# Optimization experiments

Measured on AMD Instinct MI355X. Metric: run time of the kernel, lower is better.

The kernel has to match this reference:

```python
import jax, jax.numpy as jnp
import numpy as np

NUM_HEADS = 16
ROPE_BASE = 10000.0

def rotate_half(x):
    h = x.shape[-1] // 2
    return jnp.concatenate([-x[..., h:], x[..., :h]], axis=-1)

def setup_inputs() -> dict:
    key = jax.random.key(0)
    k1, k2, k3, k4 = jax.random.split(key, 4)
    B, T, H = 2, 2048, 1024
    hidden_state = jax.random.normal(k1, (B, T, H), dtype=jnp.float32)
    # right-padding mask: per-batch valid lengths
    lengths = jnp.array([2048, 1536], dtype=jnp.int32)
    attention_mask = (jnp.arange(T, dtype=jnp.int32)[None, :] < lengths[:, None]).astype(jnp.int32)
    s = 1.0 / np.sqrt(H)
    w_qkv = jax.random.normal(k2, (H, 3 * H), dtype=jnp.float32) * s
    b_qkv = jax.random.normal(k3, (3 * H,), dtype=jnp.float32) * 0.01
    w_out = jax.random.normal(k4, (H, H), dtype=jnp.float32) * s
    return {"hidden_state": hidden_state, "attention_mask": attention_mask,
            "w_qkv": w_qkv, "b_qkv": b_qkv, "w_out": w_out}

def reference(hidden_state, attention_mask, w_qkv, b_qkv, w_out):
    B, T, H = hidden_state.shape
    hd = H // NUM_HEADS
    qkv = hidden_state @ w_qkv + b_qkv                      # [B,T,3H]
    qkv = qkv.reshape(B, T, NUM_HEADS, 3 * hd).swapaxes(1, 2)  # [B,h,T,3d]
    q, k, v = qkv[..., :hd], qkv[..., hd:2 * hd], qkv[..., 2 * hd:]
    # rotary embedding (cache computed in fp32, as in torch module)
    inv_freq = 1.0 / (ROPE_BASE ** (jnp.arange(0, hd, 2, dtype=jnp.float32) / hd))
    t = jnp.arange(T, dtype=jnp.float32)
    freqs = jnp.outer(t, inv_freq)                          # [T, hd/2]
    emb = jnp.concatenate([freqs, freqs], axis=-1)          # [T, hd]
    cos = jnp.cos(emb)[None, None]                          # [1,1,T,hd]
    sin = jnp.sin(emb)[None, None]
    q = q * cos + rotate_half(q) * sin
    k = k * cos + rotate_half(k) * sin
    scale = 1.0 / jnp.sqrt(jnp.asarray(hd, dtype=q.dtype))
    scores = jnp.einsum('bhqd,bhkd->bhqk', q, k) * scale    # [B,h,T,T]
    causal = jnp.triu(jnp.ones((T, T), dtype=bool), k=1)    # True = masked (future)
    pad = (attention_mask == 0)[:, None, None, :]           # True = masked (padded key)
    mask = causal[None, None] | pad
    scores = jnp.where(mask, jnp.finfo(scores.dtype).min, scores)
    attn = jax.nn.softmax(scores, axis=-1)
    out = jnp.einsum('bhqk,bhkd->bhqd', attn, v)            # [B,h,T,d]
    out = out.swapaxes(1, 2).reshape(B, T, H)
    return out @ w_out
```

## Files before the change

### kernel.cpp

```cpp
#include <hip/hip_runtime.h>
#include <math.h>

typedef __attribute__((ext_vector_type(8))) short short8;
typedef __attribute__((ext_vector_type(4))) short short4v;
typedef __attribute__((ext_vector_type(4))) float floatx4;

#define T_SEQ 2048
#define NHEADS 16
#define HID 1024

#if __has_builtin(__builtin_amdgcn_mfma_f32_16x16x16bf16_1k)
#define MFMA16(a,b,c) __builtin_amdgcn_mfma_f32_16x16x16bf16_1k(a,b,c,0,0,0)
#elif __has_builtin(__builtin_amdgcn_mfma_f32_16x16x16_bf16)
#define MFMA16(a,b,c) __builtin_amdgcn_mfma_f32_16x16x16_bf16(a,b,c,0,0,0)
#else
#define MFMA16(a,b,c) (c)
#endif

#if __has_builtin(__builtin_amdgcn_exp2f)
#define EXP2F(x) __builtin_amdgcn_exp2f(x)
#else
#define EXP2F(x) exp2f(x)
#endif

__device__ __forceinline__ ushort f2b(float x){
  union { float f; unsigned u; } c; c.f = x;
  unsigned r = c.u + 0x7fffu + ((c.u >> 16) & 1u);
  return (ushort)(r >> 16);
}

__device__ __forceinline__ floatx4 fzero4(){
  floatx4 v; v[0]=0.f; v[1]=0.f; v[2]=0.f; v[3]=0.f; return v;
}

__device__ __forceinline__ void gl_lds16(const ushort* g, ushort* l){
  __builtin_amdgcn_global_load_lds(
      (const __attribute__((address_space(1))) void*)g,
      (__attribute__((address_space(3))) void*)l, 16, 0, 0);
}


__global__ __launch_bounds__(256) void prep(
    const float* __restrict__ hidden, const float* __restrict__ w_qkv,
    const float* __restrict__ w_out, const int* __restrict__ amask,
    ushort* __restrict__ hO, ushort* __restrict__ wqkvT, ushort* __restrict__ woutT,
    float2* __restrict__ cs, int* __restrict__ Lb)
{
  __shared__ __align__(16) char smem[32 * 33 * 4];
  int blk = blockIdx.x;
  int tid = threadIdx.x;

  if (blk < 4096){
    int i = blk * 256 + tid;
    float4 v = ((const float4*)hidden)[i];
    ushort4 o;
    o.x = f2b(v.x); o.y = f2b(v.y); o.z = f2b(v.z); o.w = f2b(v.w);
    ((ushort4*)hO)[i] = o;
  } else if (blk < 8192){
    const float* in; ushort* out; int R, C, bx, by;
    if (blk < 7168){
      int t = blk - 4096; bx = t % 96; by = t / 96;
      in = w_qkv; out = wqkvT; R = 1024; C = 3072;
    } else {
      int t = blk - 7168; bx = t & 31; by = t >> 5;
      in = w_out; out = woutT; R = 1024; C = 1024;
    }
    float (*tile)[33] = (float(*)[33])smem;
    int c0 = bx * 32, r0 = by * 32;
    int tx = tid & 31, ty = tid >> 5;
    #pragma unroll
    for (int i = 0; i < 4; i++){
      int r = ty + i * 8;
      tile[r][tx] = in[(size_t)(r0 + r) * C + c0 + tx];
    }
    __syncthreads();
    #pragma unroll
    for (int i = 0; i < 4; i++){
      int r = ty + i * 8;
      out[(size_t)(c0 + r) * R + r0 + tx] = f2b(tile[tx][r]);
    }
  } else if (blk < 8448){
    int idx = (blk - 8192) * 256 + tid;
    int t = idx >> 5, i = idx & 31;
    float invf = powf(10000.0f, -(float)i / 32.0f);
    float a = (float)t * invf;
    cs[idx] = make_float2(cosf(a), sinf(a));
  } else {
    int b = blk - 8448;
    int* red = (int*)smem;
    int s = 0;
    for (int i = tid; i < T_SEQ; i += 256) s += amask[b * T_SEQ + i];
    red[tid] = s; __syncthreads();
    for (int o = 128; o > 0; o >>= 1){
      if (tid < o) red[tid] += red[tid + o];
      __syncthreads();
    }
    if (tid == 0) Lb[b] = red[0];
  }
}


__global__ __launch_bounds__(768, 3) void gemm_qkv(
    const ushort* __restrict__ A, const ushort* __restrict__ Bt,
    const float* __restrict__ bias,
    ushort* __restrict__ qO, ushort* __restrict__ kO, ushort* __restrict__ vT,
    const float2* __restrict__ cs)
{
  __shared__ __align__(16) ushort As[3 * 16384];
  __shared__ __align__(16) ushort Bs[2 * 12288];
  int tid = threadIdx.x;
  int bid = blockIdx.x;
  int swz = (bid & 7) * 32 + (bid >> 3);
  int bm = swz >> 4, bn = swz & 15;
  int wave = tid >> 6, lane = tid & 63;
  int wm = wave & 3, wn = wave >> 2;
  int quad = lane >> 4, l15 = lane & 15, l7 = lane & 7;

  int lr3 = lane >> 3, sl = lane & 7;
  int gsl = sl ^ lr3;
  const ushort* gA = A  + (size_t)(bm * 256 + wave * 8 + lr3) * 1024 + (gsl << 3);
  const ushort* gB = Bt + (size_t)(bn * 192 + (wave - 8) * 8 + lr3) * 1024 + (gsl << 3);

  auto stageA = [&](int slot, int kt2){
    #pragma unroll
    for (int i = 0; i < 4; i++)
      gl_lds16(gA + (size_t)(i * 64) * 1024 + kt2 * 64,
               &As[slot * 16384 + i * 4096 + wave * 512]);
  };
  auto stageB = [&](int slot, int kt2){
    #pragma unroll
    for (int i = 0; i < 6; i++)
      gl_lds16(gB + (size_t)(i * 32) * 1024 + kt2 * 64,
               &Bs[slot * 12288 + i * 2048 + (wave - 8) * 512]);
  };

  int s0 = (quad ^ l7) << 3;
  int s1 = ((quad + 4) ^ l7) << 3;

  floatx4 acc[4][4];
  #pragma unroll
  for (int i = 0; i < 4; i++)
    #pragma unroll
    for (int j = 0; j < 4; j++) acc[i][j] = fzero4();

  if (tid < 512){ stageA(0, 0); stageA(1, 1); }
  else          { stageB(0, 0); }

  int aCur = 0, aStage = 2, bCur = 0;

  for (int kt = 0; kt < 16; ++kt){
    if (tid < 512){
      if (kt < 15) asm volatile("s_waitcnt vmcnt(4)" ::: "memory");
      else         asm volatile("s_waitcnt vmcnt(0)" ::: "memory");
    } else {
      asm volatile("s_waitcnt vmcnt(0)" ::: "memory");
    }
    __builtin_amdgcn_s_barrier();

    const ushort* Ac = &As[aCur * 16384];
    const ushort* Bc = &Bs[bCur * 12288];

    short8 af[4][2], bfr[2][2];
    #pragma unroll
    for (int mt = 0; mt < 4; mt++){
      int ro = (wm * 64 + mt * 16 + l15) * 64;
      af[mt][0] = *(const short8*)&Ac[ro + s0];
      af[mt][1] = *(const short8*)&Ac[ro + s1];
    }
    #pragma unroll
    for (int nt = 0; nt < 2; nt++){
      int ro = (wn * 64 + nt * 16 + l15) * 64;
      bfr[nt][0] = *(const short8*)&Bc[ro + s0];
      bfr[nt][1] = *(const short8*)&Bc[ro + s1];
    }
    if (tid < 512){ if (kt <= 13) stageA(aStage, kt + 2); }
    else          { if (kt <= 14) stageB(bCur ^ 1, kt + 1); }

    __builtin_amdgcn_s_setprio(1);
    #pragma unroll
    for (int mt = 0; mt < 4; mt++)
      #pragma unroll
      for (int nt = 0; nt < 2; nt++){
        acc[mt][nt] = __builtin_amdgcn_mfma_f32_16x16x32_bf16(af[mt][0], bfr[nt][0], acc[mt][nt], 0, 0, 0);
        acc[mt][nt] = __builtin_amdgcn_mfma_f32_16x16x32_bf16(af[mt][1], bfr[nt][1], acc[mt][nt], 0, 0, 0);
      }
    __builtin_amdgcn_s_setprio(0);

    short8 bfr2[2][2];
    #pragma unroll
    for (int nt = 0; nt < 2; nt++){
      int ro = (wn * 64 + (nt + 2) * 16 + l15) * 64;
      bfr2[nt][0] = *(const short8*)&Bc[ro + s0];
      bfr2[nt][1] = *(const short8*)&Bc[ro + s1];
    }
    __builtin_amdgcn_s_setprio(1);
    #pragma unroll
    for (int mt = 0; mt < 4; mt++)
      #pragma unroll
      for (int nt = 0; nt < 2; nt++){
        acc[mt][nt + 2] = __builtin_amdgcn_mfma_f32_16x16x32_bf16(af[mt][0], bfr2[nt][0], acc[mt][nt + 2], 0, 0, 0);
        acc[mt][nt + 2] = __builtin_amdgcn_mfma_f32_16x16x32_bf16(af[mt][1], bfr2[nt][1], acc[mt][nt + 2], 0, 0, 0);
      }
    __builtin_amdgcn_s_setprio(0);

    aCur   = (aCur   == 2) ? 0 : aCur + 1;
    aStage = (aStage == 2) ? 0 : aStage + 1;
    bCur ^= 1;
  }

  int g = bn * 3 + wn;
  int h = g / 3, comp = g - h * 3;

  if (comp == 2){
    #pragma unroll
    for (int nt = 0; nt < 4; nt++){
      int d = nt * 16 + l15;
      float bv = bias[g * 64 + d];
      #pragma unroll
      for (int mt = 0; mt < 4; mt++){
        int row = bm * 256 + wm * 64 + mt * 16 + quad * 4;
        int t = row & (T_SEQ - 1), b_ = row >> 11;
        ushort4 o;
        o.x = f2b(acc[mt][nt][0] + bv);
        o.y = f2b(acc[mt][nt][1] + bv);
        o.z = f2b(acc[mt][nt][2] + bv);
        o.w = f2b(acc[mt][nt][3] + bv);
        *(ushort4*)&vT[(size_t)((b_ * NHEADS + h) * 64 + d) * T_SEQ + t] = o;
      }
    }
  } else {
    ushort* outP = (comp == 0) ? qO : kO;
    float qs = (comp == 0) ? 0.125f * 1.44269504089f : 1.0f;
    float bv[4], bp[4];
    #pragma unroll
    for (int nt = 0; nt < 4; nt++){
      bv[nt] = bias[g * 64 + nt * 16 + l15];
      bp[nt] = bias[g * 64 + ((nt * 16 + l15) ^ 32)];
    }
    #pragma unroll
    for (int mt = 0; mt < 4; mt++)
      #pragma unroll
      for (int r = 0; r < 4; r++){
        int row = bm * 256 + wm * 64 + mt * 16 + quad * 4 + r;
        int t = row & (T_SEQ - 1), b_ = row >> 11;
        float2 c0 = cs[t * 32 + l15];
        float2 c1 = cs[t * 32 + 16 + l15];
        size_t base = (size_t)((b_ * NHEADS + h) * T_SEQ + t) * 64 + l15;
        #pragma unroll
        for (int nt = 0; nt < 4; nt++){
          float cvv = (nt & 1) ? c1.x : c0.x;
          float svv = (nt & 1) ? c1.y : c0.y;
          float sgn = (nt < 2) ? -1.0f : 1.0f;
          float val = acc[mt][nt][r] + bv[nt];
          float pv  = acc[mt][nt ^ 2][r] + bp[nt];
          outP[base + nt * 16] = f2b((val * cvv + sgn * pv * svv) * qs);
        }
      }
  }
}


__global__ __launch_bounds__(256) void attn(
    const ushort* __restrict__ qB, const ushort* __restrict__ kB,
    const ushort* __restrict__ vTB, const int* __restrict__ Lb,
    ushort* __restrict__ oB)
{
  __shared__ __align__(16) ushort SH[2][8192];
  int tid = threadIdx.x;
  int bh = blockIdx.x;
  int qt = 31 - blockIdx.y;
  int b = bh >> 4, h = bh & 15;
  int wave = tid >> 6, lane = tid & 63;
  int quad = lane >> 4, l15 = lane & 15;
  int q0 = qt * 64;
  int L = Lb[b];

  const ushort* Qb  = qB + (size_t)bh * T_SEQ * 64;
  const ushort* Kb  = kB + (size_t)bh * T_SEQ * 64;
  const ushort* VtB = vTB + (size_t)bh * 64 * T_SEQ;

  int qrow = q0 + wave * 16 + l15;
  short8 qf0 = *(const short8*)&Qb[(size_t)qrow * 64 + quad * 8];
  short8 qf1 = *(const short8*)&Qb[(size_t)qrow * 64 + 32 + quad * 8];

  int lr = lane >> 3, ch = lane & 7;
  int sw = (ch ^ lr) * 8;
  int l7 = l15 & 7;

  float l_i = 0.f;
  floatx4 oacc[4];
  #pragma unroll
  for (int nt = 0; nt < 4; nt++) oacc[nt] = fzero4();

  int lastkb = qt;
  int lkb2 = (L - 1) >> 6;
  if (lkb2 < lastkb) lastkb = lkb2;

  auto stageKV = [&](int kb, int buf){
    int k0 = kb * 64;
    const ushort* gK = &Kb[(size_t)(k0 + wave * 16 + lr) * 64 + sw];
    gl_lds16(gK,          &SH[buf][(wave * 16) * 64]);
    gl_lds16(gK + 8 * 64, &SH[buf][(wave * 16 + 8) * 64]);
    const ushort* gV = &VtB[(size_t)(wave * 16 + lr) * T_SEQ + k0 + sw];
    gl_lds16(gV,             &SH[buf][4096 + (wave * 16) * 64]);
    gl_lds16(gV + 8 * T_SEQ, &SH[buf][4096 + (wave * 16 + 8) * 64]);
  };

  stageKV(0, 0);
  __syncthreads();

  for (int kb = 0; kb <= lastkb; ++kb){
    int cur = kb & 1;
    if (kb < lastkb) stageKV(kb + 1, cur ^ 1);
    const ushort* Ks = &SH[cur][0];
    const ushort* Vt = &SH[cur][4096];
    int k0 = kb * 64;

    floatx4 sacc[4];
    #pragma unroll
    for (int e = 0; e < 4; e++){
      short8 kf0 = *(const short8*)&Ks[(e * 16 + l15) * 64 + ((quad ^ l7) * 8)];
      short8 kf1 = *(const short8*)&Ks[(e * 16 + l15) * 64 + (((quad | 4) ^ l7) * 8)];
      floatx4 z = fzero4();
      z = __builtin_amdgcn_mfma_f32_16x16x32_bf16(kf0, qf0, z, 0, 0, 0);
      z = __builtin_amdgcn_mfma_f32_16x16x32_bf16(kf1, qf1, z, 0, 0, 0);
      sacc[e] = z;
    }

    float p[4][4];
    bool needm = (kb == qt) || (k0 + 64 > L);
    if (needm){
      #pragma unroll
      for (int e = 0; e < 4; e++)
        #pragma unroll
        for (int r = 0; r < 4; r++){
          int key = k0 + e * 16 + quad * 4 + r;
          float ev = EXP2F(sacc[e][r]);
          p[e][r] = (key <= qrow && key < L) ? ev : 0.f;
        }
    } else {
      #pragma unroll
      for (int e = 0; e < 4; e++)
        #pragma unroll
        for (int r = 0; r < 4; r++) p[e][r] = EXP2F(sacc[e][r]);
    }
    float s0 = 0.f, s1 = 0.f, s2 = 0.f, s3 = 0.f;
    #pragma unroll
    for (int e = 0; e < 4; e++){
      s0 += p[e][0]; s1 += p[e][1]; s2 += p[e][2]; s3 += p[e][3];
    }
    l_i += (s0 + s1) + (s2 + s3);

    short4v pf[4];
    #pragma unroll
    for (int e = 0; e < 4; e++){
      union { unsigned u[2]; short4v v; } pk;
      pk.u[0] = (__float_as_uint(p[e][1]) & 0xffff0000u) | (__float_as_uint(p[e][0]) >> 16);
      pk.u[1] = (__float_as_uint(p[e][3]) & 0xffff0000u) | (__float_as_uint(p[e][2]) >> 16);
      pf[e] = pk.v;
    }

    #pragma unroll
    for (int nt = 0; nt < 4; nt++){
      #pragma unroll
      for (int e = 0; e < 4; e++){
        int cw = e * 2 + (quad >> 1);
        short4v vf = *(const short4v*)&Vt[(nt * 16 + l15) * 64 + ((cw ^ l7) * 8) + (quad & 1) * 4];
        oacc[nt] = MFMA16(vf, pf[e], oacc[nt]);
      }
    }
    __syncthreads();
  }

  l_i += __shfl_xor(l_i, 16);
  l_i += __shfl_xor(l_i, 32);
  float inv = 1.f / l_i;

  ushort (*Ot)[80] = (ushort(*)[80])&SH[0][0];
  #pragma unroll
  for (int nt = 0; nt < 4; nt++){
    ushort4 o;
    o.x = f2b(oacc[nt][0] * inv);
    o.y = f2b(oacc[nt][1] * inv);
    o.z = f2b(oacc[nt][2] * inv);
    o.w = f2b(oacc[nt][3] * inv);
    *(ushort4*)&Ot[wave * 16 + l15][nt * 16 + quad * 4] = o;
  }
  __syncthreads();
  int r = tid >> 2, c = (tid & 3) * 16;
  short8 o0 = *(const short8*)&Ot[r][c];
  short8 o1 = *(const short8*)&Ot[r][c + 8];
  ushort* dst = &oB[(size_t)((b * T_SEQ + q0 + r) * NHEADS + h) * 64 + c];
  *(short8*)dst = o0;
  *(short8*)(dst + 8) = o1;
}


__global__ __launch_bounds__(256) void gemm_out_k(
    const ushort* __restrict__ A, const ushort* __restrict__ Bt,
    float* __restrict__ out)
{
  __shared__ __align__(16) ushort As[2][4096];
  __shared__ __align__(16) ushort Bs[2][2048];
  int tid = threadIdx.x;
  int bm = blockIdx.x, bn = blockIdx.y;
  int wave = tid >> 6, lane = tid & 63;
  int wm = wave >> 1, wn = wave & 1;
  int quad = lane >> 4, l15 = lane & 15;

  int lr4 = lane >> 2;
  int sc  = (lane & 3) * 8;
  const ushort* baseA = &A[(size_t)(bm * 128 + wave * 32 + lr4) * 1024 + sc];
  const ushort* baseB = &Bt[(size_t)(bn * 64 + wave * 16 + lr4) * 1024 + sc];

  floatx4 acc[4][2];
  for (int i = 0; i < 4; i++) for (int j = 0; j < 2; j++) acc[i][j] = fzero4();

  gl_lds16(baseA,             &As[0][wave * 1024]);
  gl_lds16(baseA + 16 * 1024, &As[0][wave * 1024 + 512]);
  gl_lds16(baseB,             &Bs[0][wave * 512]);
  __syncthreads();

  for (int kt = 0; kt < 32; ++kt){
    int cur = kt & 1;
    if (kt < 31){
      const ushort* gA = baseA + (kt + 1) * 32;
      const ushort* gB = baseB + (kt + 1) * 32;
      gl_lds16(gA,             &As[cur ^ 1][wave * 1024]);
      gl_lds16(gA + 16 * 1024, &As[cur ^ 1][wave * 1024 + 512]);
      gl_lds16(gB,             &Bs[cur ^ 1][wave * 512]);
    }
    short8 af[4], bfr[2];
    #pragma unroll
    for (int i = 0; i < 4; i++) af[i]  = *(const short8*)&As[cur][(wm * 64 + i * 16 + l15) * 32 + quad * 8];
    #pragma unroll
    for (int j = 0; j < 2; j++) bfr[j] = *(const short8*)&Bs[cur][(wn * 32 + j * 16 + l15) * 32 + quad * 8];
    #pragma unroll
    for (int mt = 0; mt < 4; mt++)
      #pragma unroll
      for (int nt = 0; nt < 2; nt++)
        acc[mt][nt] = __builtin_amdgcn_mfma_f32_16x16x32_bf16(af[mt], bfr[nt], acc[mt][nt], 0, 0, 0);
    __syncthreads();
  }

  #pragma unroll
  for (int nt = 0; nt < 2; nt++){
    int n = bn * 64 + wn * 32 + nt * 16 + l15;
    #pragma unroll
    for (int mt = 0; mt < 4; mt++)
      #pragma unroll
      for (int r = 0; r < 4; r++){
        int row = bm * 128 + wm * 64 + mt * 16 + quad * 4 + r;
        out[(size_t)row * 1024 + n] = acc[mt][nt][r];
      }
  }
}


extern "C" void kernel_launch(void* const* d_in, const int* in_sizes, int n_in,
                              void* d_out, int out_size, void* d_ws, size_t ws_size,
                              hipStream_t stream)
{
  const float* hidden = (const float*)d_in[0];
  const int*   amask  = (const int*)d_in[1];
  const float* w_qkv  = (const float*)d_in[2];
  const float* b_qkv  = (const float*)d_in[3];
  const float* w_out  = (const float*)d_in[4];
  float* out = (float*)d_out;

  char* ws = (char*)d_ws;
  ushort* hO    = (ushort*)(ws);
  ushort* wqkvT = (ushort*)(ws + 8388608);
  ushort* woutT = (ushort*)(ws + 14680064);
  ushort* qB    = (ushort*)(ws + 16777216);
  ushort* kB    = (ushort*)(ws + 25165824);
  ushort* vT    = (ushort*)(ws + 33554432);
  float2* cs    = (float2*)(ws + 41943040);
  int*    Lb    = (int*)(ws + 42467328);

  prep<<<8450, 256, 0, stream>>>(hidden, w_qkv, w_out, amask, hO, wqkvT, woutT, cs, Lb);
  gemm_qkv<<<dim3(256), 768, 0, stream>>>(hO, wqkvT, b_qkv, qB, kB, vT, cs);
  attn<<<dim3(32, 32), 256, 0, stream>>>(qB, kB, vT, Lb, hO );
  gemm_out_k<<<dim3(32, 16), 256, 0, stream>>>(hO, woutT, out);
}
```

Measured before the change: 167.2 us.

## Restructure output GEMM with larger tiles, triple-buffered A, swizzled LDS and grid remap

Reworks the output projection GEMM so each 512-thread block computes a 256x64 tile with a K step of 64. A is triple-buffered and B double-buffered in LDS, with explicit vmcnt waits so loads for the next steps overlap the MFMA work. An XOR swizzle on LDS columns is meant to avoid bank conflicts, and a block-index swizzle groups blocks for better cache locality. MFMA sections are wrapped in setprio. This cuts barrier count and raises arithmetic per load, but the grid shrinks from 512 to 256 blocks and LDS use per block grows.

```diff
diff --git a/kernel.cpp b/kernel.cpp
--- a/kernel.cpp
+++ b/kernel.cpp
@@ -396,51 +396,97 @@
 }
 
 
-__global__ __launch_bounds__(256) void gemm_out_k(
+__global__ __launch_bounds__(512, 2) void gemm_out_k(
     const ushort* __restrict__ A, const ushort* __restrict__ Bt,
     float* __restrict__ out)
 {
-  __shared__ __align__(16) ushort As[2][4096];
-  __shared__ __align__(16) ushort Bs[2][2048];
+  __shared__ __align__(16) ushort As[3 * 16384];
+  __shared__ __align__(16) ushort Bs[2 * 4096];
   int tid = threadIdx.x;
-  int bm = blockIdx.x, bn = blockIdx.y;
+  int bid = blockIdx.x;
+  int swz = (bid & 7) * 32 + (bid >> 3);
+  int bm = swz >> 4, bn = swz & 15;
   int wave = tid >> 6, lane = tid & 63;
   int wm = wave >> 1, wn = wave & 1;
-  int quad = lane >> 4, l15 = lane & 15;
-
-  int lr4 = lane >> 2;
-  int sc  = (lane & 3) * 8;
-  const ushort* baseA = &A[(size_t)(bm * 128 + wave * 32 + lr4) * 1024 + sc];
-  const ushort* baseB = &Bt[(size_t)(bn * 64 + wave * 16 + lr4) * 1024 + sc];
+  int quad = lane >> 4, l15 = lane & 15, l7 = lane & 7;
+
+  int lr3 = lane >> 3, sl = lane & 7;
+  int gsl = sl ^ lr3;
+  const ushort* gA = A + (size_t)(bm * 256 + wave * 8 + lr3) * 1024 + (gsl << 3);
+  int rB = tid >> 3;
+  int gslB = (tid & 7) ^ (rB & 7);
+  const ushort* gB = Bt + (size_t)(bn * 64 + rB) * 1024 + (gslB << 3);
+
+  auto stageA = [&](int slot, int kt2){
+    #pragma unroll
+    for (int i = 0; i < 4; i++)
+      gl_lds16(gA + (size_t)(i * 64) * 1024 + kt2 * 64,
+               &As[slot * 16384 + i * 4096 + wave * 512]);
+  };
+  auto stageB = [&](int slot, int kt2){
+    gl_lds16(gB + kt2 * 64, &Bs[slot * 4096 + wave * 512]);
+  };
+
+  int s0 = (quad ^ l7) << 3;
+  int s1 = ((quad + 4) ^ l7) << 3;
 
   floatx4 acc[4][2];
-  for (int i = 0; i < 4; i++) for (int j = 0; j < 2; j++) acc[i][j] = fzero4();
-
-  gl_lds16(baseA,             &As[0][wave * 1024]);
-  gl_lds16(baseA + 16 * 1024, &As[0][wave * 1024 + 512]);
-  gl_lds16(baseB,             &Bs[0][wave * 512]);
-  __syncthreads();
-
-  for (int kt = 0; kt < 32; ++kt){
-    int cur = kt & 1;
-    if (kt < 31){
-      const ushort* gA = baseA + (kt + 1) * 32;
-      const ushort* gB = baseB + (kt + 1) * 32;
-      gl_lds16(gA,             &As[cur ^ 1][wave * 1024]);
-      gl_lds16(gA + 16 * 1024, &As[cur ^ 1][wave * 1024 + 512]);
-      gl_lds16(gB,             &Bs[cur ^ 1][wave * 512]);
-    }
-    short8 af[4], bfr[2];
-    #pragma unroll
-    for (int i = 0; i < 4; i++) af[i]  = *(const short8*)&As[cur][(wm * 64 + i * 16 + l15) * 32 + quad * 8];
-    #pragma unroll
-    for (int j = 0; j < 2; j++) bfr[j] = *(const short8*)&Bs[cur][(wn * 32 + j * 16 + l15) * 32 + quad * 8];
-    #pragma unroll
-    for (int mt = 0; mt < 4; mt++)
-      #pragma unroll
-      for (int nt = 0; nt < 2; nt++)
-        acc[mt][nt] = __builtin_amdgcn_mfma_f32_16x16x32_bf16(af[mt], bfr[nt], acc[mt][nt], 0, 0, 0);
-    __syncthreads();
+  #pragma unroll
+  for (int i = 0; i < 4; i++){ acc[i][0] = fzero4(); acc[i][1] = fzero4(); }
+
+  stageB(0, 0);
+  stageA(0, 0);
+  stageA(1, 1);
+  int aCur = 0, aStage = 2, bCur = 0;
+
+  for (int kt = 0; kt < 16; ++kt){
+    if (kt < 15) asm volatile("s_waitcnt vmcnt(4)" ::: "memory");
+    else         asm volatile("s_waitcnt vmcnt(0)" ::: "memory");
+    __builtin_amdgcn_s_barrier();
+
+    const ushort* Ac = &As[aCur * 16384];
+    const ushort* Bc = &Bs[bCur * 4096];
+
+    short8 af[4][2], bf0[2], bf1[2];
+    #pragma unroll
+    for (int mt = 0; mt < 4; mt++){
+      int ro = (wm * 64 + mt * 16 + l15) * 64;
+      af[mt][0] = *(const short8*)&Ac[ro + s0];
+      af[mt][1] = *(const short8*)&Ac[ro + s1];
+    }
+    {
+      int ro = (wn * 32 + l15) * 64;
+      bf0[0] = *(const short8*)&Bc[ro + s0];
+      bf0[1] = *(const short8*)&Bc[ro + s1];
+    }
+    if (kt <= 14) stageB(bCur ^ 1, kt + 1);
+
+    __builtin_amdgcn_s_setprio(1);
+    #pragma unroll
+    for (int mt = 0; mt < 4; mt++){
+      acc[mt][0] = __builtin_amdgcn_mfma_f32_16x16x32_bf16(af[mt][0], bf0[0], acc[mt][0], 0, 0, 0);
+      acc[mt][0] = __builtin_amdgcn_mfma_f32_16x16x32_bf16(af[mt][1], bf0[1], acc[mt][0], 0, 0, 0);
+    }
+    __builtin_amdgcn_s_setprio(0);
+
+    {
+      int ro = (wn * 32 + 16 + l15) * 64;
+      bf1[0] = *(const short8*)&Bc[ro + s0];
+      bf1[1] = *(const short8*)&Bc[ro + s1];
+    }
+    if (kt <= 13) stageA(aStage, kt + 2);
+
+    __builtin_amdgcn_s_setprio(1);
+    #pragma unroll
+    for (int mt = 0; mt < 4; mt++){
+      acc[mt][1] = __builtin_amdgcn_mfma_f32_16x16x32_bf16(af[mt][0], bf1[0], acc[mt][1], 0, 0, 0);
+      acc[mt][1] = __builtin_amdgcn_mfma_f32_16x16x32_bf16(af[mt][1], bf1[1], acc[mt][1], 0, 0, 0);
+    }
+    __builtin_amdgcn_s_setprio(0);
+
+    aCur   = (aCur   == 2) ? 0 : aCur + 1;
+    aStage = (aStage == 2) ? 0 : aStage + 1;
+    bCur ^= 1;
   }
 
   #pragma unroll
@@ -450,7 +496,7 @@
     for (int mt = 0; mt < 4; mt++)
       #pragma unroll
       for (int r = 0; r < 4; r++){
-        int row = bm * 128 + wm * 64 + mt * 16 + quad * 4 + r;
+        int row = bm * 256 + wm * 64 + mt * 16 + quad * 4 + r;
         out[(size_t)row * 1024 + n] = acc[mt][nt][r];
       }
   }
@@ -481,5 +527,5 @@
   prep<<<8450, 256, 0, stream>>>(hidden, w_qkv, w_out, amask, hO, wqkvT, woutT, cs, Lb);
   gemm_qkv<<<dim3(256), 768, 0, stream>>>(hO, wqkvT, b_qkv, qB, kB, vT, cs);
   attn<<<dim3(32, 32), 256, 0, stream>>>(qB, kB, vT, Lb, hO );
-  gemm_out_k<<<dim3(32, 16), 256, 0, stream>>>(hO, woutT, out);
-}
+  gemm_out_k<<<dim3(256), 512, 0, stream>>>(hO, woutT, out);
+}
```

Result: no change. 165.7 us (-0.9%).
